# Performance work log

Hardware: AMD Instinct MI355X
Metric: run time of the kernel (lower is better)

Reference implementation:

```python
import jax, jax.numpy as jnp
import numpy as np

N_SRC = 100000
N_DST = 100000
E = 500000
D = 128      # in_units
F = 64       # efeat_dim
NB = 2       # num_basis
C = 5        # num_classes


def setup_inputs() -> dict:
    key = jax.random.key(0)
    ks = jax.random.split(key, 14)
    s = 1.0 / np.sqrt(D)
    return {
        "h_src": jax.random.normal(ks[0], (N_SRC, D), jnp.float32),
        "h_dst": jax.random.normal(ks[1], (N_DST, D), jnp.float32),
        "efeats": jax.random.normal(ks[2], (E, F), jnp.float32),
        "u_idx": jax.random.randint(ks[3], (E,), 0, N_SRC),
        "v_idx": jax.random.randint(ks[4], (E,), 0, N_DST),
        "W1": jax.random.normal(ks[5], (D, F), jnp.float32) * (1.0 / np.sqrt(F)),
        "b1": jnp.zeros((D,), jnp.float32),
        "W2": jax.random.normal(ks[6], (D, D), jnp.float32) * s,
        "b2": jnp.zeros((D,), jnp.float32),
        "W3": jax.random.normal(ks[7], (D, D), jnp.float32) * s,
        "b3": jnp.zeros((D,), jnp.float32),
        "W_comb": jax.random.normal(ks[8], (D, 2 * D), jnp.float32) * (1.0 / np.sqrt(2 * D)),
        "P": jax.random.normal(ks[9], (NB, D, D), jnp.float32) * s,
        "W_cb": jax.random.normal(ks[10], (C, NB), jnp.float32) * (1.0 / np.sqrt(NB)),
    }


def reference(h_src, h_dst, efeats, u_idx, v_idx,
              W1, b1, W2, b2, W3, b3, W_comb, P, W_cb):
    # 3-layer edge-feature MLP (dropout is identity at eval / rate=0)
    e = jax.nn.relu(efeats @ W1.T + b1)   # [E, D]
    e = jax.nn.relu(e @ W2.T + b2)        # [E, D]
    e = e @ W3.T + b3                     # [E, D]
    # gather node feats by edge endpoints, concat with transformed efeats, combine
    u = jnp.concatenate([h_src[u_idx], e], axis=1) @ W_comb.T  # [E, D]
    v = jnp.concatenate([h_dst[v_idx], e], axis=1) @ W_comb.T  # [E, D]
    # bilinear basis decode: out[e, b] = u[e] @ P[b] @ v[e]
    out = jnp.einsum('ei,bij,ej->eb', u, P, v)  # [E, NB]
    return out @ W_cb.T                          # [E, C]
```

## Files before the change

### kernel.cpp

```cpp
#include <hip/hip_runtime.h>

#define NNODE 100000
#define EDG   500000
#define DD    128
#define FF    64
#define NCLS  5

#define OFF_W1   0
#define OFF_W2   8192
#define OFF_W3   24576
#define OFF_WCR  40960
#define OFF_WCL  57344
#define OFF_P0   73728
#define OFF_P1   90112
#define OFF_HU   106496
#define OFF_HV   (106496 + NNODE * DD)
#define PREP_TOT 106496

typedef __attribute__((ext_vector_type(8))) short short8;
typedef __attribute__((ext_vector_type(4))) float f32x4;

union U4 { uint4 v; ushort s[8]; };

__device__ __forceinline__ float bf2f(ushort u) {
  return __uint_as_float(((unsigned int)u) << 16);
}
__device__ __forceinline__ ushort f2bf(float f) {
  unsigned int u = __float_as_uint(f);
  u += 0x7FFF + ((u >> 16) & 1);
  return (ushort)(u >> 16);
}

__device__ __forceinline__ void zacc(f32x4 a[2][4]) {
#pragma unroll
  for (int i = 0; i < 2; ++i)
#pragma unroll
    for (int j = 0; j < 4; ++j)
      a[i][j] = (f32x4){0.f, 0.f, 0.f, 0.f};
}

__device__ __forceinline__ void gemm_T(const ushort (*act)[136],
                                       const ushort* __restrict__ W, int K,
                                       int ksteps, f32x4 acc[2][4],
                                       int m0, int n0, int l15, int q) {
  for (int ks = 0; ks < ksteps; ++ks) {
    const int ko = ks * 32 + q * 8;
    short8 a0 = *(const short8*)(W + (m0 + l15) * K + ko);
    short8 a1 = *(const short8*)(W + (m0 + 16 + l15) * K + ko);
#pragma unroll
    for (int nt = 0; nt < 4; ++nt) {
      short8 b = *(const short8*)&act[n0 + nt * 16 + l15][ko];
      acc[0][nt] = __builtin_amdgcn_mfma_f32_16x16x32_bf16(a0, b, acc[0][nt], 0, 0, 0);
      acc[1][nt] = __builtin_amdgcn_mfma_f32_16x16x32_bf16(a1, b, acc[1][nt], 0, 0, 0);
    }
  }
}

__device__ __forceinline__ void store_T(ushort (*dst)[136], f32x4 acc[2][4],
                                        const float* __restrict__ bias, int relu,
                                        int m0, int n0, int l15, int q) {
#pragma unroll
  for (int mt = 0; mt < 2; ++mt) {
    const int feat = m0 + mt * 16 + q * 4;
    float4 bv = bias ? *(const float4*)(bias + feat) : make_float4(0.f, 0.f, 0.f, 0.f);
#pragma unroll
    for (int nt = 0; nt < 4; ++nt) {
      const int edge = n0 + nt * 16 + l15;
      float v0 = acc[mt][nt][0] + bv.x, v1 = acc[mt][nt][1] + bv.y;
      float v2 = acc[mt][nt][2] + bv.z, v3 = acc[mt][nt][3] + bv.w;
      if (relu) {
        v0 = fmaxf(v0, 0.f); v1 = fmaxf(v1, 0.f);
        v2 = fmaxf(v2, 0.f); v3 = fmaxf(v3, 0.f);
      }
      ushort4 o; o.x = f2bf(v0); o.y = f2bf(v1); o.z = f2bf(v2); o.w = f2bf(v3);
      *(ushort4*)&dst[edge][feat] = o;
    }
  }
}

__global__ void __launch_bounds__(256) prep_kernel(
    const float* __restrict__ W1, const float* __restrict__ W2,
    const float* __restrict__ W3, const float* __restrict__ W_comb,
    const float* __restrict__ P, ushort* __restrict__ ws) {
  int idx = blockIdx.x * 256 + threadIdx.x;
  if (idx >= PREP_TOT) return;
  float val;
  if (idx < 8192) {
    val = W1[idx];
  } else {
    int r = idx - 8192, m = r >> 14, rr = r & 16383;
    switch (m) {
      case 0:  val = W2[rr]; break;
      case 1:  val = W3[rr]; break;
      case 2:  { int n = rr >> 7, k = rr & 127; val = W_comb[n * 256 + 128 + k]; } break;
      case 3:  { int n = rr >> 7, k = rr & 127; val = W_comb[n * 256 + k]; } break;
      case 4:  val = P[rr]; break;
      default: val = P[16384 + rr]; break;
    }
  }
  ws[idx] = f2bf(val);
}

__global__ void __launch_bounds__(512, 4) node_kernel(
    const float* __restrict__ h_src, const float* __restrict__ h_dst,
    ushort* __restrict__ ws) {
  __shared__ ushort ACT[128][136];
  const int NT = (NNODE + 127) / 128;
  const int tid = threadIdx.x;
  const int w = tid >> 6, lane = tid & 63, l15 = lane & 15, q = lane >> 4;
  const int m0 = (w & 3) * 32, n0 = (w >> 2) * 64;
  const int bb = blockIdx.x;
  const float* h = (bb < NT) ? h_src : h_dst;
  ushort* op = ws + ((bb < NT) ? OFF_HU : OFF_HV);
  const int r0 = ((bb < NT) ? bb : bb - NT) * 128;
  const int srow = tid >> 2, part = tid & 3;
  int row = r0 + srow; if (row >= NNODE) row = NNODE - 1;
  {
    const float4* src = (const float4*)(h + (long)row * DD) + part * 8;
    ushort* d = &ACT[srow][part * 32];
#pragma unroll
    for (int i = 0; i < 8; ++i) {
      float4 v = src[i];
      ushort4 hh; hh.x = f2bf(v.x); hh.y = f2bf(v.y); hh.z = f2bf(v.z); hh.w = f2bf(v.w);
      *(ushort4*)(d + i * 4) = hh;
    }
  }
  __syncthreads();
  f32x4 acc[2][4];
  zacc(acc);
  gemm_T(ACT, ws + OFF_WCL, 128, 4, acc, m0, n0, l15, q);
  __syncthreads();
  store_T(ACT, acc, nullptr, 0, m0, n0, l15, q);
  __syncthreads();
  if (r0 + srow < NNODE) {
    const uint4* s = (const uint4*)&ACT[srow][part * 32];
    uint4* d = (uint4*)(op + (long)(r0 + srow) * DD + part * 32);
#pragma unroll
    for (int i = 0; i < 4; ++i) d[i] = s[i];
  }
}

__global__ void __launch_bounds__(512, 4) edge_kernel(
    const float* __restrict__ efeats, const int* __restrict__ u_idx,
    const int* __restrict__ v_idx, const float* __restrict__ b1,
    const float* __restrict__ b2, const float* __restrict__ b3,
    const float* __restrict__ W_cb, const ushort* __restrict__ ws,
    float* __restrict__ out) {
  __shared__ ushort ACT[128][136];
  __shared__ ushort EC[128][136];
  __shared__ float OB[128][2];

  const int tid = threadIdx.x;
  const int w = tid >> 6, lane = tid & 63;
  const int l15 = lane & 15, q = lane >> 4;
  const int m0 = (w & 3) * 32, n0 = (w >> 2) * 64;
  const long e0 = (long)blockIdx.x * 128;

  const int srow = tid >> 2, part = tid & 3;
  long grow = e0 + srow; if (grow >= EDG) grow = EDG - 1;
  const int vi = v_idx[grow], ui = u_idx[grow];

  {
    const float4* src = (const float4*)(efeats + grow * FF) + part * 4;
    ushort* d = &ACT[srow][part * 16];
#pragma unroll
    for (int i = 0; i < 4; ++i) {
      float4 v = src[i];
      ushort4 hh; hh.x = f2bf(v.x); hh.y = f2bf(v.y); hh.z = f2bf(v.z); hh.w = f2bf(v.w);
      *(ushort4*)(d + i * 4) = hh;
    }
  }
  __syncthreads();

  f32x4 acc[2][4];
  zacc(acc); gemm_T(ACT, ws + OFF_W1, 64, 2, acc, m0, n0, l15, q);
  __syncthreads(); store_T(ACT, acc, b1, 1, m0, n0, l15, q); __syncthreads();
  zacc(acc); gemm_T(ACT, ws + OFF_W2, 128, 4, acc, m0, n0, l15, q);
  __syncthreads(); store_T(ACT, acc, b2, 1, m0, n0, l15, q); __syncthreads();
  zacc(acc); gemm_T(ACT, ws + OFF_W3, 128, 4, acc, m0, n0, l15, q);
  __syncthreads(); store_T(ACT, acc, b3, 0, m0, n0, l15, q); __syncthreads();

  uint4 hvp[4];
  {
    const uint4* hp = (const uint4*)(ws + OFF_HV + (long)vi * DD + part * 32);
#pragma unroll
    for (int c = 0; c < 4; ++c) hvp[c] = hp[c];
  }
  zacc(acc); gemm_T(ACT, ws + OFF_WCR, 128, 4, acc, m0, n0, l15, q);
  __syncthreads(); store_T(EC, acc, nullptr, 0, m0, n0, l15, q); __syncthreads();

  {
#pragma unroll
    for (int c = 0; c < 4; ++c) {
      U4 a; a.v = hvp[c];
      U4 e; e.v = *(const uint4*)&EC[srow][part * 32 + c * 8];
      U4 o;
#pragma unroll
      for (int j = 0; j < 8; ++j) o.s[j] = f2bf(bf2f(a.s[j]) + bf2f(e.s[j]));
      *(uint4*)&ACT[srow][part * 32 + c * 8] = o.v;
    }
    if (tid < 256) OB[tid >> 1][tid & 1] = 0.f;
  }
  __syncthreads();

  uint4 hup[4];
  {
    const uint4* hp = (const uint4*)(ws + OFF_HU + (long)ui * DD + part * 32);
#pragma unroll
    for (int c = 0; c < 4; ++c) hup[c] = hp[c];
  }

  f32x4 tacc[2][2][4];
  zacc(tacc[0]); zacc(tacc[1]);
  for (int ks = 0; ks < 4; ++ks) {
    const int ko = ks * 32 + q * 8;
    short8 a00 = *(const short8*)(ws + OFF_P0 + (m0 + l15) * 128 + ko);
    short8 a01 = *(const short8*)(ws + OFF_P0 + (m0 + 16 + l15) * 128 + ko);
    short8 a10 = *(const short8*)(ws + OFF_P1 + (m0 + l15) * 128 + ko);
    short8 a11 = *(const short8*)(ws + OFF_P1 + (m0 + 16 + l15) * 128 + ko);
#pragma unroll
    for (int nt = 0; nt < 4; ++nt) {
      short8 b = *(const short8*)&ACT[n0 + nt * 16 + l15][ko];
      tacc[0][0][nt] = __builtin_amdgcn_mfma_f32_16x16x32_bf16(a00, b, tacc[0][0][nt], 0, 0, 0);
      tacc[0][1][nt] = __builtin_amdgcn_mfma_f32_16x16x32_bf16(a01, b, tacc[0][1][nt], 0, 0, 0);
      tacc[1][0][nt] = __builtin_amdgcn_mfma_f32_16x16x32_bf16(a10, b, tacc[1][0][nt], 0, 0, 0);
      tacc[1][1][nt] = __builtin_amdgcn_mfma_f32_16x16x32_bf16(a11, b, tacc[1][1][nt], 0, 0, 0);
    }
  }
  __syncthreads();

  {
#pragma unroll
    for (int c = 0; c < 4; ++c) {
      U4 a; a.v = hup[c];
      U4 e; e.v = *(const uint4*)&EC[srow][part * 32 + c * 8];
      U4 o;
#pragma unroll
      for (int j = 0; j < 8; ++j) o.s[j] = f2bf(bf2f(a.s[j]) + bf2f(e.s[j]));
      *(uint4*)&ACT[srow][part * 32 + c * 8] = o.v;
    }
  }
  __syncthreads();

#pragma unroll
  for (int nt = 0; nt < 4; ++nt) {
    const int edge = n0 + nt * 16 + l15;
    float pb0 = 0.f, pb1 = 0.f;
#pragma unroll
    for (int mt = 0; mt < 2; ++mt) {
      ushort4 u4 = *(const ushort4*)&ACT[edge][m0 + mt * 16 + q * 4];
      float uf;
      uf = bf2f(u4.x); pb0 += tacc[0][mt][nt][0] * uf; pb1 += tacc[1][mt][nt][0] * uf;
      uf = bf2f(u4.y); pb0 += tacc[0][mt][nt][1] * uf; pb1 += tacc[1][mt][nt][1] * uf;
      uf = bf2f(u4.z); pb0 += tacc[0][mt][nt][2] * uf; pb1 += tacc[1][mt][nt][2] * uf;
      uf = bf2f(u4.w); pb0 += tacc[0][mt][nt][3] * uf; pb1 += tacc[1][mt][nt][3] * uf;
    }
    pb0 += __shfl_xor(pb0, 16, 64); pb0 += __shfl_xor(pb0, 32, 64);
    pb1 += __shfl_xor(pb1, 16, 64); pb1 += __shfl_xor(pb1, 32, 64);
    if (q == 0) {
      atomicAdd(&OB[edge][0], pb0);
      atomicAdd(&OB[edge][1], pb1);
    }
  }
  __syncthreads();

  for (int t = tid; t < 128 * NCLS; t += 512) {
    int r = t / NCLS, c = t % NCLS;
    long erow = e0 + r;
    if (erow < EDG) {
      out[erow * NCLS + c] = OB[r][0] * W_cb[c * 2] + OB[r][1] * W_cb[c * 2 + 1];
    }
  }
}

extern "C" void kernel_launch(void* const* d_in, const int* in_sizes, int n_in,
                              void* d_out, int out_size, void* d_ws,
                              size_t ws_size, hipStream_t stream) {
  const float* h_src  = (const float*)d_in[0];
  const float* h_dst  = (const float*)d_in[1];
  const float* efeats = (const float*)d_in[2];
  const int*   u_idx  = (const int*)d_in[3];
  const int*   v_idx  = (const int*)d_in[4];
  const float* W1     = (const float*)d_in[5];
  const float* b1     = (const float*)d_in[6];
  const float* W2     = (const float*)d_in[7];
  const float* b2     = (const float*)d_in[8];
  const float* W3     = (const float*)d_in[9];
  const float* b3     = (const float*)d_in[10];
  const float* W_comb = (const float*)d_in[11];
  const float* P      = (const float*)d_in[12];
  const float* W_cb   = (const float*)d_in[13];
  ushort* ws = (ushort*)d_ws;
  float* out = (float*)d_out;

  prep_kernel<<<(PREP_TOT + 255) / 256, 256, 0, stream>>>(W1, W2, W3, W_comb, P, ws);
  node_kernel<<<2 * ((NNODE + 127) / 128), 512, 0, stream>>>(h_src, h_dst, ws);
  edge_kernel<<<(EDG + 127) / 128, 512, 0, stream>>>(efeats, u_idx, v_idx,
                                                     b1, b2, b3, W_cb, ws, out);
}
```

Measured before the change: 503.7 us.

## Ping-pong XOR-swizzled LDS buffers and use packed bf16 conversion

Replaces the padded 136-wide LDS tiles with two unpadded 128-wide buffers addressed through an XOR swizzle on 8-element chunks. GEMM stages alternate between the buffers, which removes the barrier between each GEMM and its store. Scalar float-to-bf16 rounding is replaced with the packed __float22bfloat162_rn intrinsic. LDS footprint stays about the same, and the swizzle adds some index arithmetic to every shared-memory access.

Measured after the change: 500.6 us. No clear change (-0.6%).

```diff
diff --git a/kernel.cpp b/kernel.cpp
--- a/kernel.cpp
+++ b/kernel.cpp
@@ -1,4 +1,5 @@
 #include <hip/hip_runtime.h>
+#include <hip/hip_bf16.h>
 
 #define NNODE 100000
 #define EDG   500000
@@ -30,6 +31,18 @@
   u += 0x7FFF + ((u >> 16) & 1);
   return (ushort)(u >> 16);
 }
+__device__ __forceinline__ ushort2 pk2(float a, float b) {
+  __hip_bfloat162 t = __float22bfloat162_rn(make_float2(a, b));
+  return *(ushort2*)&t;
+}
+__device__ __forceinline__ ushort4 pk4(float a, float b, float c, float d) {
+  ushort2 lo = pk2(a, b), hi = pk2(c, d);
+  ushort4 o; o.x = lo.x; o.y = lo.y; o.z = hi.x; o.w = hi.y; return o;
+}
+
+__device__ __forceinline__ int sw(int row, int col) {
+  return row * 128 + ((((col >> 3) ^ (row & 7)) << 3) | (col & 7));
+}
 
 __device__ __forceinline__ void zacc(f32x4 a[2][4]) {
 #pragma unroll
@@ -39,7 +52,7 @@
       a[i][j] = (f32x4){0.f, 0.f, 0.f, 0.f};
 }
 
-__device__ __forceinline__ void gemm_T(const ushort (*act)[136],
+__device__ __forceinline__ void gemm_T(const ushort* act,
                                        const ushort* __restrict__ W, int K,
                                        int ksteps, f32x4 acc[2][4],
                                        int m0, int n0, int l15, int q) {
@@ -49,14 +62,14 @@
     short8 a1 = *(const short8*)(W + (m0 + 16 + l15) * K + ko);
 #pragma unroll
     for (int nt = 0; nt < 4; ++nt) {
-      short8 b = *(const short8*)&act[n0 + nt * 16 + l15][ko];
+      short8 b = *(const short8*)&act[sw(n0 + nt * 16 + l15, ko)];
       acc[0][nt] = __builtin_amdgcn_mfma_f32_16x16x32_bf16(a0, b, acc[0][nt], 0, 0, 0);
       acc[1][nt] = __builtin_amdgcn_mfma_f32_16x16x32_bf16(a1, b, acc[1][nt], 0, 0, 0);
     }
   }
 }
 
-__device__ __forceinline__ void store_T(ushort (*dst)[136], f32x4 acc[2][4],
+__device__ __forceinline__ void store_T(ushort* dst, f32x4 acc[2][4],
                                         const float* __restrict__ bias, int relu,
                                         int m0, int n0, int l15, int q) {
 #pragma unroll
@@ -72,8 +85,7 @@
         v0 = fmaxf(v0, 0.f); v1 = fmaxf(v1, 0.f);
         v2 = fmaxf(v2, 0.f); v3 = fmaxf(v3, 0.f);
       }
-      ushort4 o; o.x = f2bf(v0); o.y = f2bf(v1); o.z = f2bf(v2); o.w = f2bf(v3);
-      *(ushort4*)&dst[edge][feat] = o;
+      *(ushort4*)&dst[sw(edge, feat)] = pk4(v0, v1, v2, v3);
     }
   }
 }
@@ -104,7 +116,9 @@
 __global__ void __launch_bounds__(512, 4) node_kernel(
     const float* __restrict__ h_src, const float* __restrict__ h_dst,
     ushort* __restrict__ ws) {
-  __shared__ ushort ACT[128][136];
+  __shared__ ushort BUF[2][128][128];
+  ushort* A = &BUF[0][0][0];
+  ushort* B = &BUF[1][0][0];
   const int NT = (NNODE + 127) / 128;
   const int tid = threadIdx.x;
   const int w = tid >> 6, lane = tid & 63, l15 = lane & 15, q = lane >> 4;
@@ -117,26 +131,23 @@
   int row = r0 + srow; if (row >= NNODE) row = NNODE - 1;
   {
     const float4* src = (const float4*)(h + (long)row * DD) + part * 8;
-    ushort* d = &ACT[srow][part * 32];
 #pragma unroll
     for (int i = 0; i < 8; ++i) {
       float4 v = src[i];
-      ushort4 hh; hh.x = f2bf(v.x); hh.y = f2bf(v.y); hh.z = f2bf(v.z); hh.w = f2bf(v.w);
-      *(ushort4*)(d + i * 4) = hh;
+      *(ushort4*)&A[sw(srow, part * 32 + i * 4)] = pk4(v.x, v.y, v.z, v.w);
     }
   }
   __syncthreads();
   f32x4 acc[2][4];
   zacc(acc);
-  gemm_T(ACT, ws + OFF_WCL, 128, 4, acc, m0, n0, l15, q);
-  __syncthreads();
-  store_T(ACT, acc, nullptr, 0, m0, n0, l15, q);
+  gemm_T(A, ws + OFF_WCL, 128, 4, acc, m0, n0, l15, q);
+  store_T(B, acc, nullptr, 0, m0, n0, l15, q);
   __syncthreads();
   if (r0 + srow < NNODE) {
-    const uint4* s = (const uint4*)&ACT[srow][part * 32];
     uint4* d = (uint4*)(op + (long)(r0 + srow) * DD + part * 32);
 #pragma unroll
-    for (int i = 0; i < 4; ++i) d[i] = s[i];
+    for (int i = 0; i < 4; ++i)
+      d[i] = *(const uint4*)&B[sw(srow, part * 32 + i * 8)];
   }
 }
 
@@ -146,9 +157,10 @@
     const float* __restrict__ b2, const float* __restrict__ b3,
     const float* __restrict__ W_cb, const ushort* __restrict__ ws,
     float* __restrict__ out) {
-  __shared__ ushort ACT[128][136];
-  __shared__ ushort EC[128][136];
+  __shared__ ushort BUF[2][128][128];
   __shared__ float OB[128][2];
+  ushort* A = &BUF[0][0][0];
+  ushort* B = &BUF[1][0][0];
 
   const int tid = threadIdx.x;
   const int w = tid >> 6, lane = tid & 63;
@@ -162,23 +174,24 @@
 
   {
     const float4* src = (const float4*)(efeats + grow * FF) + part * 4;
-    ushort* d = &ACT[srow][part * 16];
 #pragma unroll
     for (int i = 0; i < 4; ++i) {
       float4 v = src[i];
-      ushort4 hh; hh.x = f2bf(v.x); hh.y = f2bf(v.y); hh.z = f2bf(v.z); hh.w = f2bf(v.w);
-      *(ushort4*)(d + i * 4) = hh;
+      *(ushort4*)&A[sw(srow, part * 16 + i * 4)] = pk4(v.x, v.y, v.z, v.w);
     }
   }
   __syncthreads();
 
   f32x4 acc[2][4];
-  zacc(acc); gemm_T(ACT, ws + OFF_W1, 64, 2, acc, m0, n0, l15, q);
-  __syncthreads(); store_T(ACT, acc, b1, 1, m0, n0, l15, q); __syncthreads();
-  zacc(acc); gemm_T(ACT, ws + OFF_W2, 128, 4, acc, m0, n0, l15, q);
-  __syncthreads(); store_T(ACT, acc, b2, 1, m0, n0, l15, q); __syncthreads();
-  zacc(acc); gemm_T(ACT, ws + OFF_W3, 128, 4, acc, m0, n0, l15, q);
-  __syncthreads(); store_T(ACT, acc, b3, 0, m0, n0, l15, q); __syncthreads();
+  zacc(acc); gemm_T(A, ws + OFF_W1, 64, 2, acc, m0, n0, l15, q);
+  store_T(B, acc, b1, 1, m0, n0, l15, q);
+  __syncthreads();
+  zacc(acc); gemm_T(B, ws + OFF_W2, 128, 4, acc, m0, n0, l15, q);
+  store_T(A, acc, b2, 1, m0, n0, l15, q);
+  __syncthreads();
+  zacc(acc); gemm_T(A, ws + OFF_W3, 128, 4, acc, m0, n0, l15, q);
+  store_T(B, acc, b3, 0, m0, n0, l15, q);
+  __syncthreads();
 
   uint4 hvp[4];
   {
@@ -186,18 +199,23 @@
 #pragma unroll
     for (int c = 0; c < 4; ++c) hvp[c] = hp[c];
   }
-  zacc(acc); gemm_T(ACT, ws + OFF_WCR, 128, 4, acc, m0, n0, l15, q);
-  __syncthreads(); store_T(EC, acc, nullptr, 0, m0, n0, l15, q); __syncthreads();
+  zacc(acc); gemm_T(B, ws + OFF_WCR, 128, 4, acc, m0, n0, l15, q);
+  store_T(A, acc, nullptr, 0, m0, n0, l15, q);
+  __syncthreads();
 
   {
 #pragma unroll
     for (int c = 0; c < 4; ++c) {
       U4 a; a.v = hvp[c];
-      U4 e; e.v = *(const uint4*)&EC[srow][part * 32 + c * 8];
+      U4 e; e.v = *(const uint4*)&A[sw(srow, part * 32 + c * 8)];
       U4 o;
 #pragma unroll
-      for (int j = 0; j < 8; ++j) o.s[j] = f2bf(bf2f(a.s[j]) + bf2f(e.s[j]));
-      *(uint4*)&ACT[srow][part * 32 + c * 8] = o.v;
+      for (int j = 0; j < 8; j += 2) {
+        ushort2 p = pk2(bf2f(a.s[j]) + bf2f(e.s[j]),
+                        bf2f(a.s[j + 1]) + bf2f(e.s[j + 1]));
+        o.s[j] = p.x; o.s[j + 1] = p.y;
+      }
+      *(uint4*)&B[sw(srow, part * 32 + c * 8)] = o.v;
     }
     if (tid < 256) OB[tid >> 1][tid & 1] = 0.f;
   }
@@ -220,7 +238,7 @@
     short8 a11 = *(const short8*)(ws + OFF_P1 + (m0 + 16 + l15) * 128 + ko);
 #pragma unroll
     for (int nt = 0; nt < 4; ++nt) {
-      short8 b = *(const short8*)&ACT[n0 + nt * 16 + l15][ko];
+      short8 b = *(const short8*)&B[sw(n0 + nt * 16 + l15, ko)];
       tacc[0][0][nt] = __builtin_amdgcn_mfma_f32_16x16x32_bf16(a00, b, tacc[0][0][nt], 0, 0, 0);
       tacc[0][1][nt] = __builtin_amdgcn_mfma_f32_16x16x32_bf16(a01, b, tacc[0][1][nt], 0, 0, 0);
       tacc[1][0][nt] = __builtin_amdgcn_mfma_f32_16x16x32_bf16(a10, b, tacc[1][0][nt], 0, 0, 0);
@@ -233,11 +251,15 @@
 #pragma unroll
     for (int c = 0; c < 4; ++c) {
       U4 a; a.v = hup[c];
-      U4 e; e.v = *(const uint4*)&EC[srow][part * 32 + c * 8];
+      U4 e; e.v = *(const uint4*)&A[sw(srow, part * 32 + c * 8)];
       U4 o;
 #pragma unroll
-      for (int j = 0; j < 8; ++j) o.s[j] = f2bf(bf2f(a.s[j]) + bf2f(e.s[j]));
-      *(uint4*)&ACT[srow][part * 32 + c * 8] = o.v;
+      for (int j = 0; j < 8; j += 2) {
+        ushort2 p = pk2(bf2f(a.s[j]) + bf2f(e.s[j]),
+                        bf2f(a.s[j + 1]) + bf2f(e.s[j + 1]));
+        o.s[j] = p.x; o.s[j + 1] = p.y;
+      }
+      *(uint4*)&B[sw(srow, part * 32 + c * 8)] = o.v;
     }
   }
   __syncthreads();
@@ -248,7 +270,7 @@
     float pb0 = 0.f, pb1 = 0.f;
 #pragma unroll
     for (int mt = 0; mt < 2; ++mt) {
-      ushort4 u4 = *(const ushort4*)&ACT[edge][m0 + mt * 16 + q * 4];
+      ushort4 u4 = *(const ushort4*)&B[sw(edge, m0 + mt * 16 + q * 4)];
       float uf;
       uf = bf2f(u4.x); pb0 += tacc[0][mt][nt][0] * uf; pb1 += tacc[1][mt][nt][0] * uf;
       uf = bf2f(u4.y); pb0 += tacc[0][mt][nt][1] * uf; pb1 += tacc[1][mt][nt][1] * uf;
```

## Keep MLP activations in registers via permuted weight rows, dropping shared memory

Applied to the files above, without the earlier changes.

Weight rows and biases are permuted in the prep kernel so that each MFMA accumulator output can be packed straight into the next layer's B-operand fragment. Each wave now processes 16 edges entirely in registers, which removes the LDS staging, the block barriers and the shared-memory atomics of the old design. The node kernel is changed the same way, and the final class projection is written directly from registers. In exchange, every wave re-reads all weight tiles from global/L2 per 16 edges, and register pressure goes up (launch bounds 256,3).

Result: slower. 981.8 us (+94.9%).

```diff
diff --git a/kernel.cpp b/kernel.cpp
--- a/kernel.cpp
+++ b/kernel.cpp
@@ -1,9 +1,8 @@
 #include <hip/hip_runtime.h>
+#include <hip/hip_bf16.h>
 
 #define NNODE 100000
 #define EDG   500000
-#define DD    128
-#define FF    64
 #define NCLS  5
 
 #define OFF_W1   0
@@ -13,14 +12,14 @@
 #define OFF_WCL  57344
 #define OFF_P0   73728
 #define OFF_P1   90112
-#define OFF_HU   106496
-#define OFF_HV   (106496 + NNODE * DD)
-#define PREP_TOT 106496
+#define OFF_BIAS 106496
+#define OFF_HU   (106496 + 768)
+#define OFF_HV   (OFF_HU + NNODE * 128)
+#define W_ELEMS  106496
+#define B_ELEMS  384
 
 typedef __attribute__((ext_vector_type(8))) short short8;
 typedef __attribute__((ext_vector_type(4))) float f32x4;
-
-union U4 { uint4 v; ushort s[8]; };
 
 __device__ __forceinline__ float bf2f(ushort u) {
   return __uint_as_float(((unsigned int)u) << 16);
@@ -30,246 +29,211 @@
   u += 0x7FFF + ((u >> 16) & 1);
   return (ushort)(u >> 16);
 }
-
-__device__ __forceinline__ void zacc(f32x4 a[2][4]) {
-#pragma unroll
-  for (int i = 0; i < 2; ++i)
-#pragma unroll
-    for (int j = 0; j < 4; ++j)
-      a[i][j] = (f32x4){0.f, 0.f, 0.f, 0.f};
-}
-
-__device__ __forceinline__ void gemm_T(const ushort (*act)[136],
-                                       const ushort* __restrict__ W, int K,
-                                       int ksteps, f32x4 acc[2][4],
-                                       int m0, int n0, int l15, int q) {
-  for (int ks = 0; ks < ksteps; ++ks) {
-    const int ko = ks * 32 + q * 8;
-    short8 a0 = *(const short8*)(W + (m0 + l15) * K + ko);
-    short8 a1 = *(const short8*)(W + (m0 + 16 + l15) * K + ko);
-#pragma unroll
-    for (int nt = 0; nt < 4; ++nt) {
-      short8 b = *(const short8*)&act[n0 + nt * 16 + l15][ko];
-      acc[0][nt] = __builtin_amdgcn_mfma_f32_16x16x32_bf16(a0, b, acc[0][nt], 0, 0, 0);
-      acc[1][nt] = __builtin_amdgcn_mfma_f32_16x16x32_bf16(a1, b, acc[1][nt], 0, 0, 0);
-    }
-  }
-}
-
-__device__ __forceinline__ void store_T(ushort (*dst)[136], f32x4 acc[2][4],
-                                        const float* __restrict__ bias, int relu,
-                                        int m0, int n0, int l15, int q) {
-#pragma unroll
-  for (int mt = 0; mt < 2; ++mt) {
-    const int feat = m0 + mt * 16 + q * 4;
-    float4 bv = bias ? *(const float4*)(bias + feat) : make_float4(0.f, 0.f, 0.f, 0.f);
-#pragma unroll
-    for (int nt = 0; nt < 4; ++nt) {
-      const int edge = n0 + nt * 16 + l15;
-      float v0 = acc[mt][nt][0] + bv.x, v1 = acc[mt][nt][1] + bv.y;
-      float v2 = acc[mt][nt][2] + bv.z, v3 = acc[mt][nt][3] + bv.w;
-      if (relu) {
-        v0 = fmaxf(v0, 0.f); v1 = fmaxf(v1, 0.f);
-        v2 = fmaxf(v2, 0.f); v3 = fmaxf(v3, 0.f);
+__device__ __forceinline__ ushort2 pk2(float a, float b) {
+  __hip_bfloat162 t = __float22bfloat162_rn(make_float2(a, b));
+  return *(ushort2*)&t;
+}
+
+__device__ __forceinline__ int piperm(int p) {
+  return (p >> 5) * 32 + ((p >> 2) & 3) * 8 + ((p >> 4) & 1) * 4 + (p & 3);
+}
+
+__device__ __forceinline__ short8 pkfrag(f32x4 lo, f32x4 hi) {
+  union { short8 v; ushort2 h[4]; } o;
+  o.h[0] = pk2(lo[0], lo[1]); o.h[1] = pk2(lo[2], lo[3]);
+  o.h[2] = pk2(hi[0], hi[1]); o.h[3] = pk2(hi[2], hi[3]);
+  return o.v;
+}
+
+__device__ __forceinline__ void zero8(f32x4 a[8]) {
+#pragma unroll
+  for (int i = 0; i < 8; ++i) a[i] = (f32x4){0.f, 0.f, 0.f, 0.f};
+}
+
+template <int KS>
+__device__ __forceinline__ void gemmW(const ushort* __restrict__ W, int K,
+                                      const short8 bf[KS], f32x4 acc[8],
+                                      int l15, int q) {
+#pragma unroll
+  for (int ks = 0; ks < KS; ++ks) {
+#pragma unroll
+    for (int mt = 0; mt < 8; ++mt) {
+      short8 a = *(const short8*)(W + (mt * 16 + l15) * K + ks * 32 + q * 8);
+      acc[mt] = __builtin_amdgcn_mfma_f32_16x16x32_bf16(a, bf[ks], acc[mt], 0, 0, 0);
+    }
+  }
+}
+
+__device__ __forceinline__ void mkfrags(const f32x4 acc[8],
+                                        const float* __restrict__ bias,
+                                        int relu, short8 bf[4], int q) {
+#pragma unroll
+  for (int ks = 0; ks < 4; ++ks) {
+    f32x4 lo = acc[2 * ks], hi = acc[2 * ks + 1];
+    if (bias) {
+      float4 b0 = *(const float4*)(bias + (2 * ks) * 16 + q * 4);
+      float4 b1 = *(const float4*)(bias + (2 * ks + 1) * 16 + q * 4);
+      lo[0] += b0.x; lo[1] += b0.y; lo[2] += b0.z; lo[3] += b0.w;
+      hi[0] += b1.x; hi[1] += b1.y; hi[2] += b1.z; hi[3] += b1.w;
+    }
+    if (relu) {
+#pragma unroll
+      for (int r = 0; r < 4; ++r) {
+        lo[r] = fmaxf(lo[r], 0.f); hi[r] = fmaxf(hi[r], 0.f);
       }
-      ushort4 o; o.x = f2bf(v0); o.y = f2bf(v1); o.z = f2bf(v2); o.w = f2bf(v3);
-      *(ushort4*)&dst[edge][feat] = o;
-    }
+    }
+    bf[ks] = pkfrag(lo, hi);
   }
 }
 
 __global__ void __launch_bounds__(256) prep_kernel(
     const float* __restrict__ W1, const float* __restrict__ W2,
     const float* __restrict__ W3, const float* __restrict__ W_comb,
-    const float* __restrict__ P, ushort* __restrict__ ws) {
+    const float* __restrict__ P, const float* __restrict__ b1,
+    const float* __restrict__ b2, const float* __restrict__ b3,
+    ushort* __restrict__ ws) {
   int idx = blockIdx.x * 256 + threadIdx.x;
-  if (idx >= PREP_TOT) return;
-  float val;
-  if (idx < 8192) {
-    val = W1[idx];
-  } else {
-    int r = idx - 8192, m = r >> 14, rr = r & 16383;
-    switch (m) {
-      case 0:  val = W2[rr]; break;
-      case 1:  val = W3[rr]; break;
-      case 2:  { int n = rr >> 7, k = rr & 127; val = W_comb[n * 256 + 128 + k]; } break;
-      case 3:  { int n = rr >> 7, k = rr & 127; val = W_comb[n * 256 + k]; } break;
-      case 4:  val = P[rr]; break;
-      default: val = P[16384 + rr]; break;
-    }
-  }
-  ws[idx] = f2bf(val);
-}
-
-__global__ void __launch_bounds__(512, 4) node_kernel(
+  if (idx < W_ELEMS) {
+    float val;
+    if (idx < 8192) {
+      int p = idx >> 6, k = idx & 63;
+      val = W1[piperm(p) * 64 + k];
+    } else {
+      int r = idx - 8192, m = r >> 14, rr = r & 16383;
+      int p = rr >> 7, k = rr & 127, pp = piperm(p);
+      switch (m) {
+        case 0:  val = W2[pp * 128 + k]; break;
+        case 1:  val = W3[pp * 128 + k]; break;
+        case 2:  val = W_comb[pp * 256 + 128 + k]; break;
+        case 3:  val = W_comb[pp * 256 + k]; break;
+        case 4:  val = P[pp * 128 + k]; break;
+        default: val = P[16384 + pp * 128 + k]; break;
+      }
+    }
+    ws[idx] = f2bf(val);
+  } else if (idx < W_ELEMS + B_ELEMS) {
+    int r = idx - W_ELEMS;
+    int which = r >> 7, p = r & 127;
+    const float* src = (which == 0) ? b1 : ((which == 1) ? b2 : b3);
+    ((float*)(ws + OFF_BIAS))[r] = src[piperm(p)];
+  }
+}
+
+__global__ void __launch_bounds__(256, 3) node_kernel(
     const float* __restrict__ h_src, const float* __restrict__ h_dst,
     ushort* __restrict__ ws) {
-  __shared__ ushort ACT[128][136];
-  const int NT = (NNODE + 127) / 128;
-  const int tid = threadIdx.x;
-  const int w = tid >> 6, lane = tid & 63, l15 = lane & 15, q = lane >> 4;
-  const int m0 = (w & 3) * 32, n0 = (w >> 2) * 64;
-  const int bb = blockIdx.x;
-  const float* h = (bb < NT) ? h_src : h_dst;
-  ushort* op = ws + ((bb < NT) ? OFF_HU : OFF_HV);
-  const int r0 = ((bb < NT) ? bb : bb - NT) * 128;
-  const int srow = tid >> 2, part = tid & 3;
-  int row = r0 + srow; if (row >= NNODE) row = NNODE - 1;
-  {
-    const float4* src = (const float4*)(h + (long)row * DD) + part * 8;
-    ushort* d = &ACT[srow][part * 32];
-#pragma unroll
-    for (int i = 0; i < 8; ++i) {
-      float4 v = src[i];
-      ushort4 hh; hh.x = f2bf(v.x); hh.y = f2bf(v.y); hh.z = f2bf(v.z); hh.w = f2bf(v.w);
-      *(ushort4*)(d + i * 4) = hh;
-    }
-  }
-  __syncthreads();
-  f32x4 acc[2][4];
-  zacc(acc);
-  gemm_T(ACT, ws + OFF_WCL, 128, 4, acc, m0, n0, l15, q);
-  __syncthreads();
-  store_T(ACT, acc, nullptr, 0, m0, n0, l15, q);
-  __syncthreads();
-  if (r0 + srow < NNODE) {
-    const uint4* s = (const uint4*)&ACT[srow][part * 32];
-    uint4* d = (uint4*)(op + (long)(r0 + srow) * DD + part * 32);
-#pragma unroll
-    for (int i = 0; i < 4; ++i) d[i] = s[i];
-  }
-}
-
-__global__ void __launch_bounds__(512, 4) edge_kernel(
+  const int tid = threadIdx.x, wv = tid >> 6, lane = tid & 63;
+  const int l15 = lane & 15, q = lane >> 4;
+  long gid = (long)blockIdx.x * 4 + wv;
+  const float* h; ushort* op; long n_base;
+  if (gid < 6250) { h = h_src; op = ws + OFF_HU; n_base = gid * 16; }
+  else            { h = h_dst; op = ws + OFF_HV; n_base = (gid - 6250) * 16; }
+  const long node = n_base + l15;
+
+  short8 bx[4];
+#pragma unroll
+  for (int ks = 0; ks < 4; ++ks) {
+    const float* sp = h + node * 128 + ks * 32 + q * 8;
+    float4 x0 = *(const float4*)sp, x1 = *(const float4*)(sp + 4);
+    bx[ks] = pkfrag((f32x4){x0.x, x0.y, x0.z, x0.w},
+                    (f32x4){x1.x, x1.y, x1.z, x1.w});
+  }
+  f32x4 acc[8];
+  zero8(acc);
+  gemmW<4>(ws + OFF_WCL, 128, bx, acc, l15, q);
+#pragma unroll
+  for (int mt = 0; mt < 8; ++mt) {
+    ushort2 a = pk2(acc[mt][0], acc[mt][1]);
+    ushort2 b = pk2(acc[mt][2], acc[mt][3]);
+    ushort4 o; o.x = a.x; o.y = a.y; o.z = b.x; o.w = b.y;
+    *(ushort4*)(op + node * 128 + mt * 16 + q * 4) = o;
+  }
+}
+
+__global__ void __launch_bounds__(256, 3) edge_kernel(
     const float* __restrict__ efeats, const int* __restrict__ u_idx,
-    const int* __restrict__ v_idx, const float* __restrict__ b1,
-    const float* __restrict__ b2, const float* __restrict__ b3,
-    const float* __restrict__ W_cb, const ushort* __restrict__ ws,
-    float* __restrict__ out) {
-  __shared__ ushort ACT[128][136];
-  __shared__ ushort EC[128][136];
-  __shared__ float OB[128][2];
-
-  const int tid = threadIdx.x;
-  const int w = tid >> 6, lane = tid & 63;
+    const int* __restrict__ v_idx, const float* __restrict__ W_cb,
+    const ushort* __restrict__ ws, float* __restrict__ out) {
+  const int tid = threadIdx.x, wv = tid >> 6, lane = tid & 63;
   const int l15 = lane & 15, q = lane >> 4;
-  const int m0 = (w & 3) * 32, n0 = (w >> 2) * 64;
-  const long e0 = (long)blockIdx.x * 128;
-
-  const int srow = tid >> 2, part = tid & 3;
-  long grow = e0 + srow; if (grow >= EDG) grow = EDG - 1;
-  const int vi = v_idx[grow], ui = u_idx[grow];
-
-  {
-    const float4* src = (const float4*)(efeats + grow * FF) + part * 4;
-    ushort* d = &ACT[srow][part * 16];
-#pragma unroll
-    for (int i = 0; i < 4; ++i) {
-      float4 v = src[i];
-      ushort4 hh; hh.x = f2bf(v.x); hh.y = f2bf(v.y); hh.z = f2bf(v.z); hh.w = f2bf(v.w);
-      *(ushort4*)(d + i * 4) = hh;
-    }
-  }
-  __syncthreads();
-
-  f32x4 acc[2][4];
-  zacc(acc); gemm_T(ACT, ws + OFF_W1, 64, 2, acc, m0, n0, l15, q);
-  __syncthreads(); store_T(ACT, acc, b1, 1, m0, n0, l15, q); __syncthreads();
-  zacc(acc); gemm_T(ACT, ws + OFF_W2, 128, 4, acc, m0, n0, l15, q);
-  __syncthreads(); store_T(ACT, acc, b2, 1, m0, n0, l15, q); __syncthreads();
-  zacc(acc); gemm_T(ACT, ws + OFF_W3, 128, 4, acc, m0, n0, l15, q);
-  __syncthreads(); store_T(ACT, acc, b3, 0, m0, n0, l15, q); __syncthreads();
-
-  uint4 hvp[4];
-  {
-    const uint4* hp = (const uint4*)(ws + OFF_HV + (long)vi * DD + part * 32);
-#pragma unroll
-    for (int c = 0; c < 4; ++c) hvp[c] = hp[c];
-  }
-  zacc(acc); gemm_T(ACT, ws + OFF_WCR, 128, 4, acc, m0, n0, l15, q);
-  __syncthreads(); store_T(EC, acc, nullptr, 0, m0, n0, l15, q); __syncthreads();
-
-  {
-#pragma unroll
-    for (int c = 0; c < 4; ++c) {
-      U4 a; a.v = hvp[c];
-      U4 e; e.v = *(const uint4*)&EC[srow][part * 32 + c * 8];
-      U4 o;
-#pragma unroll
-      for (int j = 0; j < 8; ++j) o.s[j] = f2bf(bf2f(a.s[j]) + bf2f(e.s[j]));
-      *(uint4*)&ACT[srow][part * 32 + c * 8] = o.v;
-    }
-    if (tid < 256) OB[tid >> 1][tid & 1] = 0.f;
-  }
-  __syncthreads();
-
-  uint4 hup[4];
-  {
-    const uint4* hp = (const uint4*)(ws + OFF_HU + (long)ui * DD + part * 32);
-#pragma unroll
-    for (int c = 0; c < 4; ++c) hup[c] = hp[c];
-  }
-
-  f32x4 tacc[2][2][4];
-  zacc(tacc[0]); zacc(tacc[1]);
+  const float* biasp = (const float*)(ws + OFF_BIAS);
+  const long e_base = ((long)blockIdx.x * 4 + wv) * 16;
+  long eidx = e_base + l15;
+  if (eidx >= EDG) eidx = EDG - 1;
+  const int vi = v_idx[eidx], ui = u_idx[eidx];
+
+  short8 bx[2];
+#pragma unroll
+  for (int ks = 0; ks < 2; ++ks) {
+    const float* sp = efeats + eidx * 64 + ks * 32 + q * 8;
+    float4 x0 = *(const float4*)sp, x1 = *(const float4*)(sp + 4);
+    bx[ks] = pkfrag((f32x4){x0.x, x0.y, x0.z, x0.w},
+                    (f32x4){x1.x, x1.y, x1.z, x1.w});
+  }
+
+  f32x4 acc[8];
+  short8 f[4];
+  zero8(acc);
+#pragma unroll
+  for (int ks = 0; ks < 2; ++ks)
+#pragma unroll
+    for (int mt = 0; mt < 8; ++mt) {
+      short8 a = *(const short8*)(ws + OFF_W1 + (mt * 16 + l15) * 64 + ks * 32 + q * 8);
+      acc[mt] = __builtin_amdgcn_mfma_f32_16x16x32_bf16(a, bx[ks], acc[mt], 0, 0, 0);
+    }
+  mkfrags(acc, biasp, 1, f, q);
+  zero8(acc); gemmW<4>(ws + OFF_W2, 128, f, acc, l15, q);
+  mkfrags(acc, biasp + 128, 1, f, q);
+  zero8(acc); gemmW<4>(ws + OFF_W3, 128, f, acc, l15, q);
+  mkfrags(acc, biasp + 256, 0, f, q);
+  f32x4 ec[8];
+  zero8(ec); gemmW<4>(ws + OFF_WCR, 128, f, ec, l15, q);
+
+  const ushort* hvrow = ws + OFF_HV + (long)vi * 128;
+  const ushort* hurow = ws + OFF_HU + (long)ui * 128;
+  short8 V[4];
+#pragma unroll
   for (int ks = 0; ks < 4; ++ks) {
-    const int ko = ks * 32 + q * 8;
-    short8 a00 = *(const short8*)(ws + OFF_P0 + (m0 + l15) * 128 + ko);
-    short8 a01 = *(const short8*)(ws + OFF_P0 + (m0 + 16 + l15) * 128 + ko);
-    short8 a10 = *(const short8*)(ws + OFF_P1 + (m0 + l15) * 128 + ko);
-    short8 a11 = *(const short8*)(ws + OFF_P1 + (m0 + 16 + l15) * 128 + ko);
-#pragma unroll
-    for (int nt = 0; nt < 4; ++nt) {
-      short8 b = *(const short8*)&ACT[n0 + nt * 16 + l15][ko];
-      tacc[0][0][nt] = __builtin_amdgcn_mfma_f32_16x16x32_bf16(a00, b, tacc[0][0][nt], 0, 0, 0);
-      tacc[0][1][nt] = __builtin_amdgcn_mfma_f32_16x16x32_bf16(a01, b, tacc[0][1][nt], 0, 0, 0);
-      tacc[1][0][nt] = __builtin_amdgcn_mfma_f32_16x16x32_bf16(a10, b, tacc[1][0][nt], 0, 0, 0);
-      tacc[1][1][nt] = __builtin_amdgcn_mfma_f32_16x16x32_bf16(a11, b, tacc[1][1][nt], 0, 0, 0);
-    }
-  }
-  __syncthreads();
-
-  {
-#pragma unroll
-    for (int c = 0; c < 4; ++c) {
-      U4 a; a.v = hup[c];
-      U4 e; e.v = *(const uint4*)&EC[srow][part * 32 + c * 8];
-      U4 o;
-#pragma unroll
-      for (int j = 0; j < 8; ++j) o.s[j] = f2bf(bf2f(a.s[j]) + bf2f(e.s[j]));
-      *(uint4*)&ACT[srow][part * 32 + c * 8] = o.v;
-    }
-  }
-  __syncthreads();
-
-#pragma unroll
-  for (int nt = 0; nt < 4; ++nt) {
-    const int edge = n0 + nt * 16 + l15;
-    float pb0 = 0.f, pb1 = 0.f;
-#pragma unroll
-    for (int mt = 0; mt < 2; ++mt) {
-      ushort4 u4 = *(const ushort4*)&ACT[edge][m0 + mt * 16 + q * 4];
-      float uf;
-      uf = bf2f(u4.x); pb0 += tacc[0][mt][nt][0] * uf; pb1 += tacc[1][mt][nt][0] * uf;
-      uf = bf2f(u4.y); pb0 += tacc[0][mt][nt][1] * uf; pb1 += tacc[1][mt][nt][1] * uf;
-      uf = bf2f(u4.z); pb0 += tacc[0][mt][nt][2] * uf; pb1 += tacc[1][mt][nt][2] * uf;
-      uf = bf2f(u4.w); pb0 += tacc[0][mt][nt][3] * uf; pb1 += tacc[1][mt][nt][3] * uf;
-    }
-    pb0 += __shfl_xor(pb0, 16, 64); pb0 += __shfl_xor(pb0, 32, 64);
-    pb1 += __shfl_xor(pb1, 16, 64); pb1 += __shfl_xor(pb1, 32, 64);
-    if (q == 0) {
-      atomicAdd(&OB[edge][0], pb0);
-      atomicAdd(&OB[edge][1], pb1);
-    }
-  }
-  __syncthreads();
-
-  for (int t = tid; t < 128 * NCLS; t += 512) {
-    int r = t / NCLS, c = t % NCLS;
-    long erow = e0 + r;
-    if (erow < EDG) {
-      out[erow * NCLS + c] = OB[r][0] * W_cb[c * 2] + OB[r][1] * W_cb[c * 2 + 1];
-    }
+    ushort4 h0 = *(const ushort4*)(hvrow + (2 * ks) * 16 + q * 4);
+    ushort4 h1 = *(const ushort4*)(hvrow + (2 * ks + 1) * 16 + q * 4);
+    f32x4 lo, hi;
+    lo[0] = bf2f(h0.x) + ec[2 * ks][0];     lo[1] = bf2f(h0.y) + ec[2 * ks][1];
+    lo[2] = bf2f(h0.z) + ec[2 * ks][2];     lo[3] = bf2f(h0.w) + ec[2 * ks][3];
+    hi[0] = bf2f(h1.x) + ec[2 * ks + 1][0]; hi[1] = bf2f(h1.y) + ec[2 * ks + 1][1];
+    hi[2] = bf2f(h1.z) + ec[2 * ks + 1][2]; hi[3] = bf2f(h1.w) + ec[2 * ks + 1][3];
+    V[ks] = pkfrag(lo, hi);
+  }
+  f32x4 Ufp[8];
+#pragma unroll
+  for (int mt = 0; mt < 8; ++mt) {
+    ushort4 h = *(const ushort4*)(hurow + mt * 16 + q * 4);
+    Ufp[mt][0] = bf2f(h.x) + ec[mt][0];
+    Ufp[mt][1] = bf2f(h.y) + ec[mt][1];
+    Ufp[mt][2] = bf2f(h.z) + ec[mt][2];
+    Ufp[mt][3] = bf2f(h.w) + ec[mt][3];
+  }
+
+  float pb0 = 0.f, pb1 = 0.f;
+#pragma unroll
+  for (int mt = 0; mt < 8; ++mt) {
+    f32x4 t0 = {0.f, 0.f, 0.f, 0.f}, t1 = {0.f, 0.f, 0.f, 0.f};
+#pragma unroll
+    for (int ks = 0; ks < 4; ++ks) {
+      short8 a0 = *(const short8*)(ws + OFF_P0 + (mt * 16 + l15) * 128 + ks * 32 + q * 8);
+      short8 a1 = *(const short8*)(ws + OFF_P1 + (mt * 16 + l15) * 128 + ks * 32 + q * 8);
+      t0 = __builtin_amdgcn_mfma_f32_16x16x32_bf16(a0, V[ks], t0, 0, 0, 0);
+      t1 = __builtin_amdgcn_mfma_f32_16x16x32_bf16(a1, V[ks], t1, 0, 0, 0);
+    }
+    pb0 += t0[0] * Ufp[mt][0] + t0[1] * Ufp[mt][1] + t0[2] * Ufp[mt][2] + t0[3] * Ufp[mt][3];
+    pb1 += t1[0] * Ufp[mt][0] + t1[1] * Ufp[mt][1] + t1[2] * Ufp[mt][2] + t1[3] * Ufp[mt][3];
+  }
+  pb0 += __shfl_xor(pb0, 16, 64); pb0 += __shfl_xor(pb0, 32, 64);
+  pb1 += __shfl_xor(pb1, 16, 64); pb1 += __shfl_xor(pb1, 32, 64);
+
+  if (e_base + l15 < EDG) {
+    long o = (e_base + l15) * NCLS;
+    out[o + q] = pb0 * W_cb[q * 2] + pb1 * W_cb[q * 2 + 1];
+    if (q == 0) out[o + 4] = pb0 * W_cb[8] + pb1 * W_cb[9];
   }
 }
 
@@ -293,8 +257,9 @@
   ushort* ws = (ushort*)d_ws;
   float* out = (float*)d_out;
 
-  prep_kernel<<<(PREP_TOT + 255) / 256, 256, 0, stream>>>(W1, W2, W3, W_comb, P, ws);
-  node_kernel<<<2 * ((NNODE + 127) / 128), 512, 0, stream>>>(h_src, h_dst, ws);
-  edge_kernel<<<(EDG + 127) / 128, 512, 0, stream>>>(efeats, u_idx, v_idx,
-                                                     b1, b2, b3, W_cb, ws, out);
-}
+  prep_kernel<<<(W_ELEMS + B_ELEMS + 255) / 256, 256, 0, stream>>>(
+      W1, W2, W3, W_comb, P, b1, b2, b3, ws);
+  node_kernel<<<3125, 256, 0, stream>>>(h_src, h_dst, ws);
+  edge_kernel<<<(EDG / 16 + 3) / 4 + 1, 256, 0, stream>>>(
+      efeats, u_idx, v_idx, W_cb, ws, out);
+}
```
